# Optimization experiments

Measured on AMD Instinct MI355X. Metric: run time of the kernel, lower is better.

## Reference

```python
import jax, jax.numpy as jnp
import numpy as np

NUM_CLASSES = 10
K_CENTROIDS = 4
CODE_DIM = 256
BATCH = 1048576
EPS = 1e-12


def _l2_normalize(x, axis=-1):
    # matches torch F.normalize(p=2): x / max(||x||, eps)
    n = jnp.sqrt(jnp.sum(x * x, axis=axis, keepdims=True))
    return x / jnp.maximum(n, EPS)


def setup_inputs() -> dict:
    key = jax.random.key(0)
    k1, k2 = jax.random.split(key)
    # codes are L2-normalized fingerprints per the module contract
    codes = _l2_normalize(jax.random.normal(k1, (BATCH, CODE_DIM), dtype=jnp.float32))
    # centroids buffer: stored unnormalized after EMA accumulation
    centroids = 0.1 * jax.random.normal(
        k2, (NUM_CLASSES, K_CENTROIDS, CODE_DIM), dtype=jnp.float32
    )
    return {"codes": codes, "centroids": centroids}


def reference(codes, centroids):
    """_CosineCodebook.code_distance_all_classes:
    codes (B, D), centroids (C, K, D) -> (B, C) cosine distance to the
    nearest centroid of EACH class.
    """
    cents_normed = _l2_normalize(centroids, axis=-1)  # (C, K, D)
    sim = jnp.einsum("bd,ckd->bck", codes, cents_normed)  # (B, C, K)
    # min over k of (1 - sim) == 1 - max over k of sim
    dists = 1.0 - jnp.max(sim, axis=-1)  # (B, C)
    return dists
```

## Files before the change

### kernel.cpp

```cpp
#include <hip/hip_runtime.h>


typedef short short8 __attribute__((ext_vector_type(8)));
typedef float floatx4 __attribute__((ext_vector_type(4)));

#define NUM_CLASSES 10
#define DIM 256
#define NPAD 48

__device__ inline short f2bf(float f) {
  union { float f; unsigned u; } v; v.f = f;
  unsigned u = v.u;
  u += 0x7fffu + ((u >> 16) & 1u);
  return (short)(u >> 16);
}

__global__ void prep_centroids(const float* __restrict__ cents,
                               short* __restrict__ Bn) {
  int w = blockIdx.x * (blockDim.x >> 6) + (threadIdx.x >> 6);
  int lane = threadIdx.x & 63;
  if (w < 40) {
    const float4 x = *(const float4*)(cents + w * DIM + lane * 4);
    float ss = x.x * x.x + x.y * x.y + x.z * x.z + x.w * x.w;
    #pragma unroll
    for (int off = 32; off > 0; off >>= 1) ss += __shfl_xor(ss, off);
    float scale = 1.0f / fmaxf(sqrtf(ss), 1e-12f);
    short4 o;
    o.x = f2bf(x.x * scale);
    o.y = f2bf(x.y * scale);
    o.z = f2bf(x.z * scale);
    o.w = f2bf(x.w * scale);
    *(short4*)(Bn + w * DIM + lane * 4) = o;
  } else if (w < NPAD) {
    short4 z = {0, 0, 0, 0};
    *(short4*)(Bn + w * DIM + lane * 4) = z;
  }
}

__global__ __launch_bounds__(256) void dist_kernel(
    const float* __restrict__ codes, const short* __restrict__ Bn,
    float* __restrict__ out) {
  const int wave = blockIdx.x * 4 + (threadIdx.x >> 6);
  const int lane = threadIdx.x & 63;
  const int m = lane & 15;
  const int quad = lane >> 4;
  const long base = (long)wave * 16;

  const float* arow = codes + (base + m) * DIM + quad * 8;
  const short* b0 = Bn + (0 + m) * DIM + quad * 8;
  const short* b1 = Bn + (16 + m) * DIM + quad * 8;
  const short* b2 = Bn + (32 + m) * DIM + quad * 8;

  floatx4 acc0 = {0.f, 0.f, 0.f, 0.f};
  floatx4 acc1 = {0.f, 0.f, 0.f, 0.f};
  floatx4 acc2 = {0.f, 0.f, 0.f, 0.f};

  #pragma unroll
  for (int kt = 0; kt < 8; ++kt) {
    const float4 a0 = *(const float4*)(arow + kt * 32);
    const float4 a1 = *(const float4*)(arow + kt * 32 + 4);
    short8 af;
    af[0] = f2bf(a0.x); af[1] = f2bf(a0.y);
    af[2] = f2bf(a0.z); af[3] = f2bf(a0.w);
    af[4] = f2bf(a1.x); af[5] = f2bf(a1.y);
    af[6] = f2bf(a1.z); af[7] = f2bf(a1.w);
    const short8 bf0 = *(const short8*)(b0 + kt * 32);
    const short8 bf1 = *(const short8*)(b1 + kt * 32);
    const short8 bf2 = *(const short8*)(b2 + kt * 32);
    acc0 = __builtin_amdgcn_mfma_f32_16x16x32_bf16(af, bf0, acc0, 0, 0, 0);
    acc1 = __builtin_amdgcn_mfma_f32_16x16x32_bf16(af, bf1, acc1, 0, 0, 0);
    acc2 = __builtin_amdgcn_mfma_f32_16x16x32_bf16(af, bf2, acc2, 0, 0, 0);
  }

  const int cls_in = m >> 2;
  #pragma unroll
  for (int j = 0; j < 3; ++j) {
    const floatx4 a = (j == 0) ? acc0 : (j == 1) ? acc1 : acc2;
    const int cls = j * 4 + cls_in;
    #pragma unroll
    for (int r = 0; r < 4; ++r) {
      float v = a[r];
      v = fmaxf(v, __shfl_xor(v, 1));
      v = fmaxf(v, __shfl_xor(v, 2));
      if ((lane & 3) == 0 && cls < NUM_CLASSES) {
        const long row = base + quad * 4 + r;
        out[row * NUM_CLASSES + cls] = 1.0f - v;
      }
    }
  }
}

extern "C" void kernel_launch(void* const* d_in, const int* in_sizes, int n_in,
                              void* d_out, int out_size, void* d_ws,
                              size_t ws_size, hipStream_t stream) {
  const float* codes = (const float*)d_in[0];
  const float* cents = (const float*)d_in[1];
  float* out = (float*)d_out;
  short* Bn = (short*)d_ws;

  const int batch = in_sizes[0] / DIM;
  const int tiles = batch / 16;
  const int blocks = tiles / 4;

  prep_centroids<<<dim3(12), dim3(256), 0, stream>>>(cents, Bn);
  dist_kernel<<<dim3(blocks), dim3(256), 0, stream>>>(codes, Bn, out);
}
```

Measured before the change: 1.429 ms.

## Fuse centroid normalization into distance kernel and stage centroids in swizzled LDS

Removes the separate centroid-prep kernel and its workspace buffer. Each block now reads the 40 raw centroids, L2-normalizes them, converts them to bf16 and writes them into shared memory with an XOR swizzle before the MFMA loop. B fragments then come from LDS instead of global memory. This saves a kernel launch and turns repeated global B loads into bank-conflict-avoiding LDS reads. The cost is that every block redoes the normalization and reads 40 KB of fp32 centroids, and must wait at a __syncthreads barrier.

```diff
diff --git a/kernel.cpp b/kernel.cpp
--- a/kernel.cpp
+++ b/kernel.cpp
@@ -15,41 +15,45 @@
   return (short)(u >> 16);
 }
 
-__global__ void prep_centroids(const float* __restrict__ cents,
-                               short* __restrict__ Bn) {
-  int w = blockIdx.x * (blockDim.x >> 6) + (threadIdx.x >> 6);
-  int lane = threadIdx.x & 63;
-  if (w < 40) {
-    const float4 x = *(const float4*)(cents + w * DIM + lane * 4);
-    float ss = x.x * x.x + x.y * x.y + x.z * x.z + x.w * x.w;
-    #pragma unroll
-    for (int off = 32; off > 0; off >>= 1) ss += __shfl_xor(ss, off);
-    float scale = 1.0f / fmaxf(sqrtf(ss), 1e-12f);
-    short4 o;
-    o.x = f2bf(x.x * scale);
-    o.y = f2bf(x.y * scale);
-    o.z = f2bf(x.z * scale);
-    o.w = f2bf(x.w * scale);
-    *(short4*)(Bn + w * DIM + lane * 4) = o;
-  } else if (w < NPAD) {
-    short4 z = {0, 0, 0, 0};
-    *(short4*)(Bn + w * DIM + lane * 4) = z;
+__global__ __launch_bounds__(256) void dist_kernel(
+    const float* __restrict__ codes, const float* __restrict__ cents,
+    float* __restrict__ out) {
+  __shared__ short Bn[NPAD * DIM];
+
+  const int wid = threadIdx.x >> 6;
+  const int lane = threadIdx.x & 63;
+
+  #pragma unroll
+  for (int i = 0; i < 12; ++i) {
+    const int r = wid * 12 + i;
+    short4 o = {0, 0, 0, 0};
+    if (r < 40) {
+      const float4 x = *(const float4*)(cents + r * DIM + lane * 4);
+      float ss = x.x * x.x + x.y * x.y + x.z * x.z + x.w * x.w;
+      #pragma unroll
+      for (int off = 32; off > 0; off >>= 1) ss += __shfl_xor(ss, off);
+      const float scale = 1.0f / fmaxf(sqrtf(ss), 1e-12f);
+      o.x = f2bf(x.x * scale);
+      o.y = f2bf(x.y * scale);
+      o.z = f2bf(x.z * scale);
+      o.w = f2bf(x.w * scale);
+    }
+    *(short4*)(&Bn[r * DIM + ((lane * 4) ^ ((r & 7) << 3))]) = o;
   }
-}
+  __syncthreads();
 
-__global__ __launch_bounds__(256) void dist_kernel(
-    const float* __restrict__ codes, const short* __restrict__ Bn,
-    float* __restrict__ out) {
-  const int wave = blockIdx.x * 4 + (threadIdx.x >> 6);
-  const int lane = threadIdx.x & 63;
+  const int wave = blockIdx.x * 4 + wid;
   const int m = lane & 15;
   const int quad = lane >> 4;
   const long base = (long)wave * 16;
 
   const float* arow = codes + (base + m) * DIM + quad * 8;
-  const short* b0 = Bn + (0 + m) * DIM + quad * 8;
-  const short* b1 = Bn + (16 + m) * DIM + quad * 8;
-  const short* b2 = Bn + (32 + m) * DIM + quad * 8;
+
+  const int qq = quad ^ (m & 3);
+  const int kx = (m >> 2) & 1;
+  const short* lb0 = Bn + (m + 0) * DIM + qq * 8;
+  const short* lb1 = lb0 + 16 * DIM;
+  const short* lb2 = lb0 + 32 * DIM;
 
   floatx4 acc0 = {0.f, 0.f, 0.f, 0.f};
   floatx4 acc1 = {0.f, 0.f, 0.f, 0.f};
@@ -64,9 +68,10 @@
     af[2] = f2bf(a0.z); af[3] = f2bf(a0.w);
     af[4] = f2bf(a1.x); af[5] = f2bf(a1.y);
     af[6] = f2bf(a1.z); af[7] = f2bf(a1.w);
-    const short8 bf0 = *(const short8*)(b0 + kt * 32);
-    const short8 bf1 = *(const short8*)(b1 + kt * 32);
-    const short8 bf2 = *(const short8*)(b2 + kt * 32);
+    const int ko = ((kt ^ kx) << 5);
+    const short8 bf0 = *(const short8*)(lb0 + ko);
+    const short8 bf1 = *(const short8*)(lb1 + ko);
+    const short8 bf2 = *(const short8*)(lb2 + ko);
     acc0 = __builtin_amdgcn_mfma_f32_16x16x32_bf16(af, bf0, acc0, 0, 0, 0);
     acc1 = __builtin_amdgcn_mfma_f32_16x16x32_bf16(af, bf1, acc1, 0, 0, 0);
     acc2 = __builtin_amdgcn_mfma_f32_16x16x32_bf16(af, bf2, acc2, 0, 0, 0);
@@ -96,12 +101,11 @@
   const float* codes = (const float*)d_in[0];
   const float* cents = (const float*)d_in[1];
   float* out = (float*)d_out;
-  short* Bn = (short*)d_ws;
+  (void)d_ws; (void)ws_size;
 
   const int batch = in_sizes[0] / DIM;
   const int tiles = batch / 16;
   const int blocks = tiles / 4;
 
-  prep_centroids<<<dim3(12), dim3(256), 0, stream>>>(cents, Bn);
-  dist_kernel<<<dim3(blocks), dim3(256), 0, stream>>>(codes, Bn, out);
+  dist_kernel<<<dim3(blocks), dim3(256), 0, stream>>>(codes, cents, out);
 }
```

Result: no change. 1.412 ms (-1.2%).
